# Kernel optimization log

Hardware: AMD Instinct MI355X
Metric: run time of the kernel (lower is better)

## Reference

```python
import jax, jax.numpy as jnp
import numpy as np


def setup_inputs() -> dict:
    key = jax.random.key(0)
    k1, k2, k3 = jax.random.split(key, 3)
    B, gd, gh, gw = 4, 8, 16, 16
    H, W = 1024, 1024
    grid = jax.random.normal(k1, (B, 12, gd, gh, gw), dtype=jnp.float32)
    guide = jax.random.uniform(k2, (B, H, W), dtype=jnp.float32)
    image = jax.random.uniform(k3, (B, 3, H, W), dtype=jnp.float32)
    return {"grid": grid, "guide": guide, "image": image}


def _slice_apply(grid, guide, image):
    # grid: [B, 12, gd, gh, gw]; guide: [B, H, W] in [0,1]; image: [B, 3, H, W]
    B, C, gd, gh, gw = grid.shape
    _, h, w = guide.shape
    dt = grid.dtype
    # continuous grid coordinates (Halide reference convention)
    gx = (jnp.arange(w, dtype=dt) + 0.5) * gw / w          # [w]
    gy = (jnp.arange(h, dtype=dt) + 0.5) * gh / h          # [h]
    gz = guide * gd                                        # [B,h,w]
    fx = jnp.floor(gx - 0.5)
    fy = jnp.floor(gy - 0.5)
    fz = jnp.floor(gz - 0.5)
    bidx = jnp.arange(B)[:, None, None]
    coeffs = jnp.zeros((B, h, w, C), dt)
    # 8-corner trilinear gather with tent weights (clamped borders)
    for dz in (0, 1):
        zf = fz + dz
        wz = jnp.maximum(1.0 - jnp.abs(zf + 0.5 - gz), 0.0)       # [B,h,w]
        iz = jnp.clip(zf, 0, gd - 1).astype(jnp.int32)
        for dy in (0, 1):
            yf = fy + dy
            wy = jnp.maximum(1.0 - jnp.abs(yf + 0.5 - gy), 0.0)   # [h]
            iy = jnp.clip(yf, 0, gh - 1).astype(jnp.int32)
            for dx in (0, 1):
                xf = fx + dx
                wx = jnp.maximum(1.0 - jnp.abs(xf + 0.5 - gx), 0.0)  # [w]
                ix = jnp.clip(xf, 0, gw - 1).astype(jnp.int32)
                # gather -> [B,h,w,C]
                g = grid[bidx, :, iz, iy[None, :, None], ix[None, None, :]]
                wgt = wz * wy[None, :, None] * wx[None, None, :]
                coeffs = coeffs + g * wgt[..., None]
    # per-pixel 3x4 affine transform: out_i = sum_j A_ij * in_j + b_i
    co = coeffs.reshape(B, h, w, 3, 4)
    out = jnp.einsum('bhwij,bjhw->bihw', co[..., :3], image) + co[..., 3].transpose(0, 3, 1, 2)
    return out


def reference(grid, guide, image):
    return _slice_apply(grid, guide, image)
```

## Files before the change

### kernel.cpp

```cpp
#include <hip/hip_runtime.h>

#define IMH 1024
#define IMW 1024
#define GD 8
#define GH 16
#define GW 16
#define NC 12

__global__ __launch_bounds__(256) void bsa_kernel(
    const float* __restrict__ grid,
    const float* __restrict__ guide,
    const float* __restrict__ image,
    float* __restrict__ out)
{
    const int y = blockIdx.x;
    const int b = blockIdx.y;

    __shared__ __align__(16) float sG[GD][GW][NC];

    const float gy  = (y + 0.5f) * ((float)GH / IMH);
    const float fyf = floorf(gy - 0.5f);
    const float ty  = gy - 0.5f - fyf;
    const int   fy  = (int)fyf;
    const int   iy0 = min(GH - 1, max(0, fy));
    const int   iy1 = min(GH - 1, max(0, fy + 1));

    const float* gb = grid + (size_t)b * NC * GD * GH * GW;
    for (int i = threadIdx.x; i < GD * GW * NC; i += 256) {
        const int c = i % NC;
        const int x = (i / NC) % GW;
        const int z = i / (NC * GW);
        const float v0 = gb[((c * GD + z) * GH + iy0) * GW + x];
        const float v1 = gb[((c * GD + z) * GH + iy1) * GW + x];
        sG[z][x][c] = v0 + ty * (v1 - v0);
    }
    __syncthreads();

    const int x0 = threadIdx.x * 4;
    const size_t plane = (size_t)IMH * IMW;

    const float* gp = guide + ((size_t)b * IMH + y) * IMW + x0;
    const float* ip = image + ((size_t)b * 3 * IMH + y) * IMW + x0;

    const float4 gv = *(const float4*)gp;
    const float4 ir = *(const float4*)(ip);
    const float4 ig = *(const float4*)(ip + plane);
    const float4 ib = *(const float4*)(ip + 2 * plane);

    const float gvals[4] = {gv.x, gv.y, gv.z, gv.w};
    const float rv[4]    = {ir.x, ir.y, ir.z, ir.w};
    const float gv2[4]   = {ig.x, ig.y, ig.z, ig.w};
    const float bv[4]    = {ib.x, ib.y, ib.z, ib.w};

    float o0[4], o1[4], o2[4];

#pragma unroll
    for (int p = 0; p < 4; ++p) {
        const int x = x0 + p;
        const float gx  = (x + 0.5f) * ((float)GW / IMW);
        const float fxf = floorf(gx - 0.5f);
        const float tx  = gx - 0.5f - fxf;
        const int   fx  = (int)fxf;
        const int   ix0 = min(GW - 1, max(0, fx));
        const int   ix1 = min(GW - 1, max(0, fx + 1));

        const float gz  = gvals[p] * (float)GD;
        const float fzf = floorf(gz - 0.5f);
        const float tz  = gz - 0.5f - fzf;
        const int   fzi = (int)fzf;
        const int   iz0 = min(GD - 1, max(0, fzi));
        const int   iz1 = min(GD - 1, max(0, fzi + 1));

        const float w00 = (1.0f - tz) * (1.0f - tx);
        const float w01 = (1.0f - tz) * tx;
        const float w10 = tz * (1.0f - tx);
        const float w11 = tz * tx;

        const float* p00 = &sG[iz0][ix0][0];
        const float* p01 = &sG[iz0][ix1][0];
        const float* p10 = &sG[iz1][ix0][0];
        const float* p11 = &sG[iz1][ix1][0];

        float res[3];
#pragma unroll
        for (int i = 0; i < 3; ++i) {
            const float4 a = *(const float4*)(p00 + 4 * i);
            const float4 c = *(const float4*)(p01 + 4 * i);
            const float4 d = *(const float4*)(p10 + 4 * i);
            const float4 e = *(const float4*)(p11 + 4 * i);
            const float c0 = w00 * a.x + w01 * c.x + w10 * d.x + w11 * e.x;
            const float c1 = w00 * a.y + w01 * c.y + w10 * d.y + w11 * e.y;
            const float c2 = w00 * a.z + w01 * c.z + w10 * d.z + w11 * e.z;
            const float c3 = w00 * a.w + w01 * c.w + w10 * d.w + w11 * e.w;
            res[i] = c0 * rv[p] + c1 * gv2[p] + c2 * bv[p] + c3;
        }
        o0[p] = res[0];
        o1[p] = res[1];
        o2[p] = res[2];
    }

    float* op = out + ((size_t)b * 3 * IMH + y) * IMW + x0;
    *(float4*)(op)             = make_float4(o0[0], o0[1], o0[2], o0[3]);
    *(float4*)(op + plane)     = make_float4(o1[0], o1[1], o1[2], o1[3]);
    *(float4*)(op + 2 * plane) = make_float4(o2[0], o2[1], o2[2], o2[3]);
}

extern "C" void kernel_launch(void* const* d_in, const int* in_sizes, int n_in,
                              void* d_out, int out_size, void* d_ws, size_t ws_size,
                              hipStream_t stream) {
    const float* grid  = (const float*)d_in[0];
    const float* guide = (const float*)d_in[1];
    const float* image = (const float*)d_in[2];
    float* out = (float*)d_out;

    const int B = in_sizes[1] / (IMH * IMW);
    dim3 g(IMH, B);
    bsa_kernel<<<g, 256, 0, stream>>>(grid, guide, image, out);
}
```

Before: 131.4 us.

## Transpose shared grid to x-major and switch to strided per-pixel access

Reorders the shared-memory slice to [x][z][c] and changes the fill loop to read the global grid with x fastest, so global loads during the fill are contiguous. Each thread now processes pixels spaced 256 apart with scalar loads and stores instead of four adjacent pixels with float4 accesses. With the new mapping, neighbouring lanes in a wavefront share the same grid x cell, which makes their LDS reads land on the same addresses. The cost is losing 128-bit global vector loads and stores, which may leave more memory instructions in flight.

Result: faster. 118.8 us (-9.6%).

```diff
diff --git a/kernel.cpp b/kernel.cpp
--- a/kernel.cpp
+++ b/kernel.cpp
@@ -16,7 +16,7 @@
     const int y = blockIdx.x;
     const int b = blockIdx.y;
 
-    __shared__ __align__(16) float sG[GD][GW][NC];
+    __shared__ __align__(16) float sG[GW][GD][NC];
 
     const float gy  = (y + 0.5f) * ((float)GH / IMH);
     const float fyf = floorf(gy - 0.5f);
@@ -27,36 +27,29 @@
 
     const float* gb = grid + (size_t)b * NC * GD * GH * GW;
     for (int i = threadIdx.x; i < GD * GW * NC; i += 256) {
-        const int c = i % NC;
-        const int x = (i / NC) % GW;
-        const int z = i / (NC * GW);
+        const int x = i & (GW - 1);
+        const int z = (i >> 4) & (GD - 1);
+        const int c = i >> 7;
         const float v0 = gb[((c * GD + z) * GH + iy0) * GW + x];
         const float v1 = gb[((c * GD + z) * GH + iy1) * GW + x];
-        sG[z][x][c] = v0 + ty * (v1 - v0);
+        sG[x][z][c] = v0 + ty * (v1 - v0);
     }
     __syncthreads();
 
-    const int x0 = threadIdx.x * 4;
     const size_t plane = (size_t)IMH * IMW;
-
-    const float* gp = guide + ((size_t)b * IMH + y) * IMW + x0;
-    const float* ip = image + ((size_t)b * 3 * IMH + y) * IMW + x0;
-
-    const float4 gv = *(const float4*)gp;
-    const float4 ir = *(const float4*)(ip);
-    const float4 ig = *(const float4*)(ip + plane);
-    const float4 ib = *(const float4*)(ip + 2 * plane);
-
-    const float gvals[4] = {gv.x, gv.y, gv.z, gv.w};
-    const float rv[4]    = {ir.x, ir.y, ir.z, ir.w};
-    const float gv2[4]   = {ig.x, ig.y, ig.z, ig.w};
-    const float bv[4]    = {ib.x, ib.y, ib.z, ib.w};
-
-    float o0[4], o1[4], o2[4];
+    const float* gp = guide + ((size_t)b * IMH + y) * IMW;
+    const float* ip = image + ((size_t)b * 3 * IMH + y) * IMW;
+    float*       op = out   + ((size_t)b * 3 * IMH + y) * IMW;
 
 #pragma unroll
     for (int p = 0; p < 4; ++p) {
-        const int x = x0 + p;
+        const int x = threadIdx.x + 256 * p;
+
+        const float gv = gp[x];
+        const float rv = ip[x];
+        const float g2 = ip[x + plane];
+        const float bv = ip[x + 2 * plane];
+
         const float gx  = (x + 0.5f) * ((float)GW / IMW);
         const float fxf = floorf(gx - 0.5f);
         const float tx  = gx - 0.5f - fxf;
@@ -64,7 +57,7 @@
         const int   ix0 = min(GW - 1, max(0, fx));
         const int   ix1 = min(GW - 1, max(0, fx + 1));
 
-        const float gz  = gvals[p] * (float)GD;
+        const float gz  = gv * (float)GD;
         const float fzf = floorf(gz - 0.5f);
         const float tz  = gz - 0.5f - fzf;
         const int   fzi = (int)fzf;
@@ -76,10 +69,10 @@
         const float w10 = tz * (1.0f - tx);
         const float w11 = tz * tx;
 
-        const float* p00 = &sG[iz0][ix0][0];
-        const float* p01 = &sG[iz0][ix1][0];
-        const float* p10 = &sG[iz1][ix0][0];
-        const float* p11 = &sG[iz1][ix1][0];
+        const float* p00 = &sG[ix0][iz0][0];
+        const float* p01 = &sG[ix1][iz0][0];
+        const float* p10 = &sG[ix0][iz1][0];
+        const float* p11 = &sG[ix1][iz1][0];
 
         float res[3];
 #pragma unroll
@@ -92,17 +85,13 @@
             const float c1 = w00 * a.y + w01 * c.y + w10 * d.y + w11 * e.y;
             const float c2 = w00 * a.z + w01 * c.z + w10 * d.z + w11 * e.z;
             const float c3 = w00 * a.w + w01 * c.w + w10 * d.w + w11 * e.w;
-            res[i] = c0 * rv[p] + c1 * gv2[p] + c2 * bv[p] + c3;
+            res[i] = c0 * rv + c1 * g2 + c2 * bv + c3;
         }
-        o0[p] = res[0];
-        o1[p] = res[1];
-        o2[p] = res[2];
+
+        op[x]             = res[0];
+        op[x + plane]     = res[1];
+        op[x + 2 * plane] = res[2];
     }
-
-    float* op = out + ((size_t)b * 3 * IMH + y) * IMW + x0;
-    *(float4*)(op)             = make_float4(o0[0], o0[1], o0[2], o0[3]);
-    *(float4*)(op + plane)     = make_float4(o1[0], o1[1], o1[2], o1[3]);
-    *(float4*)(op + 2 * plane) = make_float4(o2[0], o2[1], o2[2], o2[3]);
 }
 
 extern "C" void kernel_launch(void* const* d_in, const int* in_sizes, int n_in,
```
